# Optimization experiments

Measured on AMD Instinct MI355X. Metric: run time of the kernel, lower is better.

## Reference

```python
import jax, jax.numpy as jnp
import numpy as np

EMB_DIM = 1024
NUM_HEADS = 16
HEAD_DIM = EMB_DIM // NUM_HEADS
B, S = 4, 1024


def _split_heads(x):
    # [B, S, E] -> [B, H, S, E/H]
    b, s, e = x.shape
    return x.reshape(b, s, NUM_HEADS, e // NUM_HEADS).transpose(0, 2, 1, 3)


def _merge_heads(x):
    # [B, H, S, D] -> [B, S, H*D]
    b, h, s, d = x.shape
    return x.transpose(0, 2, 1, 3).reshape(b, s, h * d)


def setup_inputs() -> dict:
    key = jax.random.key(0)
    ks = jax.random.split(key, 8)
    w_scale = 0.02
    return {
        "Re": jax.random.normal(ks[0], (B, S, EMB_DIM), jnp.float32),
        "Im": jax.random.normal(ks[1], (B, S, EMB_DIM), jnp.float32),
        "pos_enc": jax.random.normal(ks[2], (B, S, HEAD_DIM), jnp.float32),
        "Wq": jax.random.normal(ks[3], (EMB_DIM, EMB_DIM), jnp.float32) * w_scale,
        "bq": jnp.zeros((EMB_DIM,), jnp.float32),
        "Wk": jax.random.normal(ks[4], (EMB_DIM, EMB_DIM), jnp.float32) * w_scale,
        "bk": jnp.zeros((EMB_DIM,), jnp.float32),
        "Wv": jax.random.normal(ks[5], (EMB_DIM, EMB_DIM), jnp.float32) * w_scale,
        "bv": jnp.zeros((EMB_DIM,), jnp.float32),
        "Wo": jax.random.normal(ks[6], (EMB_DIM, EMB_DIM), jnp.float32) * w_scale,
        "bo": jnp.zeros((EMB_DIM,), jnp.float32),
    }


def reference(Re, Im, pos_enc, Wq, bq, Wk, bk, Wv, bv, Wo, bo):
    # projections + head split
    Q = _split_heads(Re @ Wq + bq)          # [B,H,S,D]
    K = _split_heads(Re @ Wk + bk)          # [B,H,S,D]
    ImH = _split_heads(Im)                  # [B,H,S,D]
    P = pos_enc[:, None, :, :]              # [B,1,S,D] broadcast over heads
    Q = Q + P
    K = K + P
    # real part of (Q + i*Im)(K - i*Im)^T = Q K^T + Im Im^T
    denom = jnp.sqrt(jnp.asarray(EMB_DIM, Q.dtype))  # NOTE: sqrt(emb_dim), as in source
    scores = (jnp.einsum("bhqd,bhkd->bhqk", Q, K)
              + jnp.einsum("bhqd,bhkd->bhqk", ImH, ImH)) / denom
    weights = jax.nn.softmax(scores, axis=-1)
    V = _split_heads(Re @ Wv + bv) + P      # value_pos_enc=True
    out = jnp.einsum("bhqk,bhkd->bhqd", weights, V)
    return _merge_heads(out) @ Wo + bo
```

## Files before the change

kernel.cpp:

```cpp
#include <hip/hip_runtime.h>
#include <hip/hip_bf16.h>
#include <stdint.h>

#define BATCH 4
#define SEQ   1024
#define EMB   1024
#define NHEAD 16
#define HDIM  64
#define MTOT  (BATCH*SEQ)
#define MELEM (MTOT*EMB)

typedef __attribute__((ext_vector_type(8))) short short8;
typedef __attribute__((ext_vector_type(4))) float f32x4;
typedef __attribute__((ext_vector_type(4))) unsigned short us4;

static __device__ __forceinline__ short f2bf(float f) {
  __hip_bfloat16 h = __float2bfloat16(f);
  return __builtin_bit_cast(short, h);
}

static __device__ __forceinline__ void cp16(const void* g, const void* lds_uniform) {
  __builtin_amdgcn_global_load_lds(
      (const __attribute__((address_space(1))) unsigned int*)(uintptr_t)g,
      (__attribute__((address_space(3))) unsigned int*)(unsigned int)(uintptr_t)lds_uniform,
      16, 0, 0);
}

__global__ __launch_bounds__(256) void cvt_bf16(const float* __restrict__ in0,
                                                const float* __restrict__ in1,
                                                short* __restrict__ out0,
                                                short* __restrict__ out1) {
  const float* in  = blockIdx.y ? in1  : in0;
  short*       out = blockIdx.y ? out1 : out0;
  int i = blockIdx.x * 256 + threadIdx.x;
  float4 f = ((const float4*)in)[i];
  union { unsigned short u[4]; uint2 v; } r;
  r.u[0] = (unsigned short)f2bf(f.x);
  r.u[1] = (unsigned short)f2bf(f.y);
  r.u[2] = (unsigned short)f2bf(f.z);
  r.u[3] = (unsigned short)f2bf(f.w);
  ((uint2*)out)[i] = r.v;
}

__global__ __launch_bounds__(256) void wtrans(const float* __restrict__ W0,
                                              const float* __restrict__ W1,
                                              const float* __restrict__ W2,
                                              const float* __restrict__ W3,
                                              short* __restrict__ WtBase) {
  const int z = blockIdx.z;
  const float* W = (z == 0) ? W0 : (z == 1) ? W1 : (z == 2) ? W2 : W3;
  short* Wt = WtBase + (size_t)z * EMB * EMB;
  __shared__ short tile[32][33];
  int nT = blockIdx.x * 32, kT = blockIdx.y * 32;
  int tx = threadIdx.x, ty = threadIdx.y;
  #pragma unroll
  for (int i = 0; i < 4; ++i)
    tile[ty + 8*i][tx] = f2bf(W[(size_t)(kT + ty + 8*i) * EMB + nT + tx]);
  __syncthreads();
  #pragma unroll
  for (int i = 0; i < 4; ++i)
    Wt[(size_t)(nT + ty + 8*i) * EMB + kT + tx] = tile[tx][ty + 8*i];
}

template <bool HAS_P, bool OUT_F32>
__global__ __launch_bounds__(256) void gemm_bt(const short* __restrict__ A,
                                               const short* __restrict__ WtBase,
                                               const float* __restrict__ b0,
                                               const float* __restrict__ b1,
                                               const float* __restrict__ b2,
                                               const float* __restrict__ pos,
                                               void* __restrict__ outBase,
                                               short* __restrict__ vtOut) {
  const int z = blockIdx.z;
  const short* Bt = WtBase + (size_t)z * EMB * EMB;
  const float* bias = (z == 0) ? b0 : (z == 1 ? b1 : b2);
  const int m0 = blockIdx.y * 128, n0 = blockIdx.x * 128;

  __shared__ __align__(16) short As[128 * 64];
  __shared__ __align__(16) short Bs[128 * 64];

  const int t = threadIdx.x;
  const int lane = t & 63, w = t >> 6;
  const int wm = w >> 1, wn = w & 1;
  const int quad = lane >> 4, l16 = lane & 15;
  const int lrow8 = lane >> 3, lchunk = lane & 7;
  const int gch = lchunk ^ lrow8;
  const int sw7 = l16 & 7;

  const short* Arow = A  + (size_t)(m0 + w * 32 + lrow8) * EMB + gch * 8;
  const short* Brow = Bt + (size_t)(n0 + w * 32 + lrow8) * EMB + gch * 8;

  f32x4 acc[4][4] = {};

  for (int k0 = 0; k0 < EMB; k0 += 64) {
    #pragma unroll
    for (int s = 0; s < 4; ++s) {
      cp16(Arow + (size_t)(s * 8) * EMB + k0, &As[(w * 32 + s * 8) * 64]);
      cp16(Brow + (size_t)(s * 8) * EMB + k0, &Bs[(w * 32 + s * 8) * 64]);
    }
    __syncthreads();
    #pragma unroll
    for (int ks = 0; ks < 2; ++ks) {
      const int chv = ((ks << 2) + quad) ^ sw7;
      short8 af[4], bfr[4];
      #pragma unroll
      for (int i = 0; i < 4; ++i)
        af[i] = *(const short8*)&As[(wm * 64 + i * 16 + l16) * 64 + chv * 8];
      #pragma unroll
      for (int j = 0; j < 4; ++j)
        bfr[j] = *(const short8*)&Bs[(wn * 64 + j * 16 + l16) * 64 + chv * 8];
      #pragma unroll
      for (int i = 0; i < 4; ++i)
        #pragma unroll
        for (int j = 0; j < 4; ++j)
          acc[i][j] = __builtin_amdgcn_mfma_f32_16x16x32_bf16(af[i], bfr[j], acc[i][j], 0, 0, 0);
    }
    __syncthreads();
  }

  #pragma unroll
  for (int i = 0; i < 4; ++i) {
    int mbase = m0 + wm * 64 + i * 16 + quad * 4;
    #pragma unroll
    for (int j = 0; j < 4; ++j) {
      int n = n0 + wn * 64 + j * 16 + l16;
      float bn = bias[n];
      if (HAS_P && z == 2) {
        int bh = (mbase >> 10) * NHEAD + (n >> 6);
        int d = n & (HDIM - 1);
        int s = mbase & (SEQ - 1);
        us4 pk;
        #pragma unroll
        for (int r = 0; r < 4; ++r) {
          float v = acc[i][j][r] + bn + pos[(size_t)(mbase + r) * HDIM + d];
          pk[r] = (unsigned short)f2bf(v);
        }
        *(us4*)&vtOut[((size_t)bh * HDIM + d) * SEQ + s] = pk;
      } else {
        #pragma unroll
        for (int r = 0; r < 4; ++r) {
          int mm = mbase + r;
          float v = acc[i][j][r] + bn;
          if (HAS_P) v += pos[(size_t)mm * HDIM + (n & (HDIM - 1))];
          size_t oidx = (size_t)z * MELEM + (size_t)mm * EMB + n;
          if (OUT_F32) ((float*)outBase)[oidx] = v;
          else         ((short*)outBase)[oidx] = f2bf(v);
        }
      }
    }
  }
}

#define PWS 68
__global__ __launch_bounds__(256) void attn(const short* __restrict__ Qp,
                                            const short* __restrict__ Kp,
                                            const short* __restrict__ VtG,
                                            const short* __restrict__ Imb,
                                            short* __restrict__ attnA) {
  const int qb = blockIdx.y * 64;
  const int bh = blockIdx.x;
  const int b = bh >> 4, h = bh & 15;
  const int t = threadIdx.x, lane = t & 63, w = t >> 6;
  const int quad = lane >> 4, l16 = lane & 15;
  const int lrow8 = lane >> 3, lchunk = lane & 7;
  const int gch = lchunk ^ lrow8;
  const int sw7 = l16 & 7;

  __shared__ __align__(16) short tiles[3 * 64 * 64];
  __shared__ __align__(16) short Pw[4 * 16 * PWS];

  const int q = qb + w * 16 + l16;
  const size_t qoff = ((size_t)(b * SEQ + q)) * EMB + h * HDIM + quad * 8;
  short8 aq[2], aim[2];
  aq[0]  = *(const short8*)&Qp [qoff];
  aq[1]  = *(const short8*)&Qp [qoff + 32];
  aim[0] = *(const short8*)&Imb[qoff];
  aim[1] = *(const short8*)&Imb[qoff + 32];

  float lr[4] = {0.f, 0.f, 0.f, 0.f};
  f32x4 o[4] = {};

  const float SC = 0.03125f * 1.44269504089f;
  const size_t kimBase = ((size_t)b * SEQ) * EMB + h * HDIM + gch * 8;
  const size_t vtBase  = ((size_t)bh * HDIM) * SEQ + gch * 8;
  const int I0 = w * 6;

  for (int kt = 0; kt < 16; ++kt) {
    const int kBase = kt * 64;
    __syncthreads();
    #pragma unroll
    for (int s = 0; s < 6; ++s) {
      const int I = I0 + s;
      const int tz = I >> 3;
      const int row = ((I & 7) * 8) + lrow8;
      const short* g;
      if (tz == 0)      g = Kp  + kimBase + (size_t)(kBase + row) * EMB;
      else if (tz == 1) g = Imb + kimBase + (size_t)(kBase + row) * EMB;
      else              g = VtG + vtBase + (size_t)row * SEQ + kBase;
      cp16(g, &tiles[I * 512]);
    }
    __syncthreads();

    f32x4 sa[4] = {};
    #pragma unroll
    for (int c = 0; c < 4; ++c) {
      const int rowoff = (c * 16 + l16) * 64;
      #pragma unroll
      for (int st = 0; st < 2; ++st) {
        const int chv = (((st << 2) + quad) ^ sw7) * 8;
        short8 bk = *(const short8*)&tiles[rowoff + chv];
        short8 bi = *(const short8*)&tiles[4096 + rowoff + chv];
        sa[c] = __builtin_amdgcn_mfma_f32_16x16x32_bf16(aq [st], bk, sa[c], 0, 0, 0);
        sa[c] = __builtin_amdgcn_mfma_f32_16x16x32_bf16(aim[st], bi, sa[c], 0, 0, 0);
      }
    }

    short* pw = &Pw[w * 16 * PWS];
    #pragma unroll
    for (int c = 0; c < 4; ++c) {
      #pragma unroll
      for (int r = 0; r < 4; ++r) {
        float p = exp2f(sa[c][r] * SC);
        lr[r] += p;
        pw[(quad * 4 + r) * PWS + c * 16 + l16] = f2bf(p);
      }
    }

    short8 ap[2];
    ap[0] = *(const short8*)&pw[l16 * PWS + quad * 8];
    ap[1] = *(const short8*)&pw[l16 * PWS + 32 + quad * 8];
    #pragma unroll
    for (int cd = 0; cd < 4; ++cd) {
      const int rowoff = 8192 + (cd * 16 + l16) * 64;
      #pragma unroll
      for (int st = 0; st < 2; ++st) {
        short8 bv2 = *(const short8*)&tiles[rowoff + (((st << 2) + quad) ^ sw7) * 8];
        o[cd] = __builtin_amdgcn_mfma_f32_16x16x32_bf16(ap[st], bv2, o[cd], 0, 0, 0);
      }
    }
  }

  #pragma unroll
  for (int r = 0; r < 4; ++r) {
    #pragma unroll
    for (int msk = 1; msk < 16; msk <<= 1) lr[r] += __shfl_xor(lr[r], msk);
  }
  #pragma unroll
  for (int r = 0; r < 4; ++r) {
    int qq = qb + w * 16 + quad * 4 + r;
    float inv = 1.f / lr[r];
    size_t base = ((size_t)(b * SEQ + qq)) * EMB + h * HDIM;
    #pragma unroll
    for (int cd = 0; cd < 4; ++cd)
      attnA[base + cd * 16 + l16] = f2bf(o[cd][r] * inv);
  }
}

extern "C" void kernel_launch(void* const* d_in, const int* in_sizes, int n_in,
                              void* d_out, int out_size, void* d_ws, size_t ws_size,
                              hipStream_t stream) {
  const float* Re  = (const float*)d_in[0];
  const float* Im  = (const float*)d_in[1];
  const float* pos = (const float*)d_in[2];
  const float* Wq  = (const float*)d_in[3];
  const float* bq  = (const float*)d_in[4];
  const float* Wk  = (const float*)d_in[5];
  const float* bk  = (const float*)d_in[6];
  const float* Wv  = (const float*)d_in[7];
  const float* bv  = (const float*)d_in[8];
  const float* Wo  = (const float*)d_in[9];
  const float* bo  = (const float*)d_in[10];

  short* ws    = (short*)d_ws;
  short* Rebf  = ws;
  short* Imbf  = ws + (size_t)MELEM;
  short* Wt    = ws + (size_t)2 * MELEM;
  short* Qp    = ws + (size_t)3 * MELEM;
  short* Kp    = Qp + (size_t)MELEM;
  short* VtG   = Qp + (size_t)2 * MELEM;
  short* attnA = ws + (size_t)6 * MELEM;

  cvt_bf16<<<dim3(MELEM / 1024, 2), 256, 0, stream>>>(Re, Im, Rebf, Imbf);

  wtrans<<<dim3(32, 32, 4), dim3(32, 8), 0, stream>>>(Wq, Wk, Wv, Wo, Wt);

  gemm_bt<true, false><<<dim3(EMB / 128, MTOT / 128, 3), 256, 0, stream>>>(
      Rebf, Wt, bq, bk, bv, pos, Qp, VtG);

  attn<<<dim3(BATCH * NHEAD, SEQ / 64), 256, 0, stream>>>(
      Qp, Kp, VtG, Imbf, attnA);

  gemm_bt<false, true><<<dim3(EMB / 128, MTOT / 128, 1), 256, 0, stream>>>(
      attnA, Wt + 3 * EMB * EMB, bo, bo, bo, nullptr, d_out, nullptr);
}
```

Before: 232.9 us.

## Double query rows per attention wave, add narrower-tile output GEMM, faster bf16 rounding

```diff
diff --git a/kernel.cpp b/kernel.cpp
--- a/kernel.cpp
+++ b/kernel.cpp
@@ -14,9 +14,9 @@
 typedef __attribute__((ext_vector_type(4))) float f32x4;
 typedef __attribute__((ext_vector_type(4))) unsigned short us4;
 
-static __device__ __forceinline__ short f2bf(float f) {
-  __hip_bfloat16 h = __float2bfloat16(f);
-  return __builtin_bit_cast(short, h);
+static __device__ __forceinline__ unsigned short f2bf_fast(float f) {
+  unsigned u = __builtin_bit_cast(unsigned, f);
+  return (unsigned short)((u + 0x8000u) >> 16);
 }
 
 static __device__ __forceinline__ void cp16(const void* g, const void* lds_uniform) {
@@ -34,12 +34,9 @@
   short*       out = blockIdx.y ? out1 : out0;
   int i = blockIdx.x * 256 + threadIdx.x;
   float4 f = ((const float4*)in)[i];
-  union { unsigned short u[4]; uint2 v; } r;
-  r.u[0] = (unsigned short)f2bf(f.x);
-  r.u[1] = (unsigned short)f2bf(f.y);
-  r.u[2] = (unsigned short)f2bf(f.z);
-  r.u[3] = (unsigned short)f2bf(f.w);
-  ((uint2*)out)[i] = r.v;
+  unsigned r0 = ((unsigned)f2bf_fast(f.y) << 16) | f2bf_fast(f.x);
+  unsigned r1 = ((unsigned)f2bf_fast(f.w) << 16) | f2bf_fast(f.z);
+  ((uint2*)out)[i] = make_uint2(r0, r1);
 }
 
 __global__ __launch_bounds__(256) void wtrans(const float* __restrict__ W0,
@@ -55,7 +52,7 @@
   int tx = threadIdx.x, ty = threadIdx.y;
   #pragma unroll
   for (int i = 0; i < 4; ++i)
-    tile[ty + 8*i][tx] = f2bf(W[(size_t)(kT + ty + 8*i) * EMB + nT + tx]);
+    tile[ty + 8*i][tx] = (short)f2bf_fast(W[(size_t)(kT + ty + 8*i) * EMB + nT + tx]);
   __syncthreads();
   #pragma unroll
   for (int i = 0; i < 4; ++i)
@@ -133,7 +130,7 @@
         #pragma unroll
         for (int r = 0; r < 4; ++r) {
           float v = acc[i][j][r] + bn + pos[(size_t)(mbase + r) * HDIM + d];
-          pk[r] = (unsigned short)f2bf(v);
+          pk[r] = f2bf_fast(v);
         }
         *(us4*)&vtOut[((size_t)bh * HDIM + d) * SEQ + s] = pk;
       } else {
@@ -144,20 +141,83 @@
           if (HAS_P) v += pos[(size_t)mm * HDIM + (n & (HDIM - 1))];
           size_t oidx = (size_t)z * MELEM + (size_t)mm * EMB + n;
           if (OUT_F32) ((float*)outBase)[oidx] = v;
-          else         ((short*)outBase)[oidx] = f2bf(v);
+          else         ((short*)outBase)[oidx] = (short)f2bf_fast(v);
         }
       }
     }
   }
 }
 
+__global__ __launch_bounds__(256) void gemm_wo(const short* __restrict__ A,
+                                               const short* __restrict__ Bt,
+                                               const float* __restrict__ bias,
+                                               float* __restrict__ out) {
+  const int m0 = blockIdx.y * 128, n0 = blockIdx.x * 64;
+
+  __shared__ __align__(16) short As[128 * 64];
+  __shared__ __align__(16) short Bs[64 * 64];
+
+  const int t = threadIdx.x;
+  const int lane = t & 63, w = t >> 6;
+  const int wm = w >> 1, wn = w & 1;
+  const int quad = lane >> 4, l16 = lane & 15;
+  const int lrow8 = lane >> 3, lchunk = lane & 7;
+  const int gch = lchunk ^ lrow8;
+  const int sw7 = l16 & 7;
+
+  const short* Arow = A  + (size_t)(m0 + w * 32 + lrow8) * EMB + gch * 8;
+  const short* Brow = Bt + (size_t)(n0 + w * 16 + lrow8) * EMB + gch * 8;
+
+  f32x4 acc[4][2] = {};
+
+  for (int k0 = 0; k0 < EMB; k0 += 64) {
+    #pragma unroll
+    for (int s = 0; s < 4; ++s)
+      cp16(Arow + (size_t)(s * 8) * EMB + k0, &As[(w * 32 + s * 8) * 64]);
+    #pragma unroll
+    for (int s = 0; s < 2; ++s)
+      cp16(Brow + (size_t)(s * 8) * EMB + k0, &Bs[(w * 16 + s * 8) * 64]);
+    __syncthreads();
+    #pragma unroll
+    for (int ks = 0; ks < 2; ++ks) {
+      const int chv = ((ks << 2) + quad) ^ sw7;
+      short8 af[4], bfr[2];
+      #pragma unroll
+      for (int i = 0; i < 4; ++i)
+        af[i] = *(const short8*)&As[(wm * 64 + i * 16 + l16) * 64 + chv * 8];
+      #pragma unroll
+      for (int j = 0; j < 2; ++j)
+        bfr[j] = *(const short8*)&Bs[(wn * 32 + j * 16 + l16) * 64 + chv * 8];
+      #pragma unroll
+      for (int i = 0; i < 4; ++i)
+        #pragma unroll
+        for (int j = 0; j < 2; ++j)
+          acc[i][j] = __builtin_amdgcn_mfma_f32_16x16x32_bf16(af[i], bfr[j], acc[i][j], 0, 0, 0);
+    }
+    __syncthreads();
+  }
+
+  #pragma unroll
+  for (int i = 0; i < 4; ++i) {
+    int mbase = m0 + wm * 64 + i * 16 + quad * 4;
+    #pragma unroll
+    for (int j = 0; j < 2; ++j) {
+      int n = n0 + wn * 32 + j * 16 + l16;
+      float bn = bias[n];
+      #pragma unroll
+      for (int r = 0; r < 4; ++r)
+        out[(size_t)(mbase + r) * EMB + n] = acc[i][j][r] + bn;
+    }
+  }
+}
+
 #define PWS 68
-__global__ __launch_bounds__(256) void attn(const short* __restrict__ Qp,
-                                            const short* __restrict__ Kp,
-                                            const short* __restrict__ VtG,
-                                            const short* __restrict__ Imb,
-                                            short* __restrict__ attnA) {
-  const int qb = blockIdx.y * 64;
+__global__ __launch_bounds__(256, 4) void attn(const short* __restrict__ Qp,
+                                               const short* __restrict__ Kp,
+                                               const short* __restrict__ VtG,
+                                               const short* __restrict__ Imb,
+                                               short* __restrict__ attnA) {
+  const int qb = blockIdx.y * 128;
   const int bh = blockIdx.x;
   const int b = bh >> 4, h = bh & 15;
   const int t = threadIdx.x, lane = t & 63, w = t >> 6;
@@ -169,16 +229,19 @@
   __shared__ __align__(16) short tiles[3 * 64 * 64];
   __shared__ __align__(16) short Pw[4 * 16 * PWS];
 
-  const int q = qb + w * 16 + l16;
-  const size_t qoff = ((size_t)(b * SEQ + q)) * EMB + h * HDIM + quad * 8;
-  short8 aq[2], aim[2];
-  aq[0]  = *(const short8*)&Qp [qoff];
-  aq[1]  = *(const short8*)&Qp [qoff + 32];
-  aim[0] = *(const short8*)&Imb[qoff];
-  aim[1] = *(const short8*)&Imb[qoff + 32];
-
-  float lr[4] = {0.f, 0.f, 0.f, 0.f};
-  f32x4 o[4] = {};
+  short8 aq[2][2], aim[2][2];
+  #pragma unroll
+  for (int g = 0; g < 2; ++g) {
+    const int q = qb + w * 32 + g * 16 + l16;
+    const size_t qoff = ((size_t)(b * SEQ + q)) * EMB + h * HDIM + quad * 8;
+    aq [g][0] = *(const short8*)&Qp [qoff];
+    aq [g][1] = *(const short8*)&Qp [qoff + 32];
+    aim[g][0] = *(const short8*)&Imb[qoff];
+    aim[g][1] = *(const short8*)&Imb[qoff + 32];
+  }
+
+  float lr[2][4] = {};
+  f32x4 o[2][4] = {};
 
   const float SC = 0.03125f * 1.44269504089f;
   const size_t kimBase = ((size_t)b * SEQ) * EMB + h * HDIM + gch * 8;
@@ -201,7 +264,7 @@
     }
     __syncthreads();
 
-    f32x4 sa[4] = {};
+    f32x4 sa[2][4] = {};
     #pragma unroll
     for (int c = 0; c < 4; ++c) {
       const int rowoff = (c * 16 + l16) * 64;
@@ -210,49 +273,57 @@
         const int chv = (((st << 2) + quad) ^ sw7) * 8;
         short8 bk = *(const short8*)&tiles[rowoff + chv];
         short8 bi = *(const short8*)&tiles[4096 + rowoff + chv];
-        sa[c] = __builtin_amdgcn_mfma_f32_16x16x32_bf16(aq [st], bk, sa[c], 0, 0, 0);
-        sa[c] = __builtin_amdgcn_mfma_f32_16x16x32_bf16(aim[st], bi, sa[c], 0, 0, 0);
+        #pragma unroll
+        for (int g = 0; g < 2; ++g) {
+          sa[g][c] = __builtin_amdgcn_mfma_f32_16x16x32_bf16(aq [g][st], bk, sa[g][c], 0, 0, 0);
+          sa[g][c] = __builtin_amdgcn_mfma_f32_16x16x32_bf16(aim[g][st], bi, sa[g][c], 0, 0, 0);
+        }
       }
     }
 
     short* pw = &Pw[w * 16 * PWS];
-    #pragma unroll
-    for (int c = 0; c < 4; ++c) {
-      #pragma unroll
-      for (int r = 0; r < 4; ++r) {
-        float p = exp2f(sa[c][r] * SC);
-        lr[r] += p;
-        pw[(quad * 4 + r) * PWS + c * 16 + l16] = f2bf(p);
+    short8 ap[2][2];
+    #pragma unroll
+    for (int g = 0; g < 2; ++g) {
+      #pragma unroll
+      for (int c = 0; c < 4; ++c) {
+        #pragma unroll
+        for (int r = 0; r < 4; ++r) {
+          float p = __builtin_amdgcn_exp2f(sa[g][c][r] * SC);
+          lr[g][r] += p;
+          pw[(quad * 4 + r) * PWS + c * 16 + l16] = (short)f2bf_fast(p);
+        }
       }
-    }
-
-    short8 ap[2];
-    ap[0] = *(const short8*)&pw[l16 * PWS + quad * 8];
-    ap[1] = *(const short8*)&pw[l16 * PWS + 32 + quad * 8];
+      ap[g][0] = *(const short8*)&pw[l16 * PWS + quad * 8];
+      ap[g][1] = *(const short8*)&pw[l16 * PWS + 32 + quad * 8];
+    }
+
     #pragma unroll
     for (int cd = 0; cd < 4; ++cd) {
       const int rowoff = 8192 + (cd * 16 + l16) * 64;
       #pragma unroll
       for (int st = 0; st < 2; ++st) {
         short8 bv2 = *(const short8*)&tiles[rowoff + (((st << 2) + quad) ^ sw7) * 8];
-        o[cd] = __builtin_amdgcn_mfma_f32_16x16x32_bf16(ap[st], bv2, o[cd], 0, 0, 0);
+        #pragma unroll
+        for (int g = 0; g < 2; ++g)
+          o[g][cd] = __builtin_amdgcn_mfma_f32_16x16x32_bf16(ap[g][st], bv2, o[g][cd], 0, 0, 0);
       }
     }
   }
 
   #pragma unroll
-  for (int r = 0; r < 4; ++r) {
-    #pragma unroll
-    for (int msk = 1; msk < 16; msk <<= 1) lr[r] += __shfl_xor(lr[r], msk);
-  }
-  #pragma unroll
-  for (int r = 0; r < 4; ++r) {
-    int qq = qb + w * 16 + quad * 4 + r;
-    float inv = 1.f / lr[r];
-    size_t base = ((size_t)(b * SEQ + qq)) * EMB + h * HDIM;
-    #pragma unroll
-    for (int cd = 0; cd < 4; ++cd)
-      attnA[base + cd * 16 + l16] = f2bf(o[cd][r] * inv);
+  for (int g = 0; g < 2; ++g) {
+    #pragma unroll
+    for (int r = 0; r < 4; ++r) {
+      #pragma unroll
+      for (int msk = 1; msk < 16; msk <<= 1) lr[g][r] += __shfl_xor(lr[g][r], msk);
+      int qq = qb + w * 32 + g * 16 + quad * 4 + r;
+      float inv = 1.f / lr[g][r];
+      size_t base = ((size_t)(b * SEQ + qq)) * EMB + h * HDIM;
+      #pragma unroll
+      for (int cd = 0; cd < 4; ++cd)
+        attnA[base + cd * 16 + l16] = (short)f2bf_fast(o[g][cd][r] * inv);
+    }
   }
 }
 
@@ -287,9 +358,9 @@
   gemm_bt<true, false><<<dim3(EMB / 128, MTOT / 128, 3), 256, 0, stream>>>(
       Rebf, Wt, bq, bk, bv, pos, Qp, VtG);
 
-  attn<<<dim3(BATCH * NHEAD, SEQ / 64), 256, 0, stream>>>(
+  attn<<<dim3(BATCH * NHEAD, SEQ / 128), 256, 0, stream>>>(
       Qp, Kp, VtG, Imbf, attnA);
 
-  gemm_bt<false, true><<<dim3(EMB / 128, MTOT / 128, 1), 256, 0, stream>>>(
-      attnA, Wt + 3 * EMB * EMB, bo, bo, bo, nullptr, d_out, nullptr);
-}
+  gemm_wo<<<dim3(EMB / 64, MTOT / 128), 256, 0, stream>>>(
+      attnA, Wt + 3 * EMB * EMB, bo, (float*)d_out);
+}
```

Measured after the change: 258.4 us. 11.0% more time.
